# Optimization experiments

Measured on AMD Instinct MI355X. Metric: run time of the kernel, lower is better.

## Reference

```python
import jax, jax.numpy as jnp
import numpy as np
from jax import lax

B, P, K = 16, 1024, 32          # clouds, points per cloud, kNN neighbors
N = B * P
NCLS = 40
DIMS = [3, 64, 128, 256]


def setup_inputs() -> dict:
    key = jax.random.key(0)
    ks = jax.random.split(key, 16)
    inp = {
        "x": jax.random.normal(ks[0], (N, DIMS[0]), dtype=jnp.float32),
        "batch": jnp.repeat(jnp.arange(B, dtype=jnp.int64), P),
        "target": jax.random.randint(ks[1], (N,), 0, NCLS, dtype=jnp.int64),
    }
    for i, (fi, fo) in enumerate(zip(DIMS[:-1], DIMS[1:])):
        scale = 1.0 / np.sqrt(2 * fi)
        inp[f"W{i+1}"] = jax.random.normal(ks[2 + 2 * i], (2 * fi, fo), dtype=jnp.float32) * scale
        inp[f"b{i+1}"] = jnp.zeros((fo,), dtype=jnp.float32)
    inp["Wc"] = jax.random.normal(ks[10], (DIMS[-1], NCLS), dtype=jnp.float32) * (1.0 / np.sqrt(DIMS[-1]))
    inp["bc"] = jnp.zeros((NCLS,), dtype=jnp.float32)
    return inp


def knn_graph(x):
    """Per-cloud kNN (loop=False). x: [N,F] with nodes grouped in B clouds of P.
    Returns global neighbor indices [N, K]."""
    xb = x.reshape(B, P, -1)
    sq = jnp.sum(xb * xb, axis=-1)                       # [B,P]
    d2 = sq[:, :, None] + sq[:, None, :] - 2.0 * jnp.einsum("bpf,bqf->bpq", xb, xb)
    d2 = d2 + jnp.eye(P, dtype=x.dtype) * jnp.finfo(x.dtype).max  # exclude self-loops
    _, idx = lax.top_k(-d2, K)                           # [B,P,K] local indices
    gidx = idx + (jnp.arange(B) * P)[:, None, None]      # local -> global node ids
    return gidx.reshape(N, K)


def edge_conv(x, nbr, W, b):
    """EdgeConv: max_j MLP([x_i, x_j - x_i])."""
    xj = x[nbr]                                          # [N,K,F] gather
    xi = x[:, None, :]
    feat = jnp.concatenate([jnp.broadcast_to(xi, xj.shape), xj - xi], axis=-1)  # [N,K,2F]
    h = jnp.einsum("nkf,fo->nko", feat, W) + b           # [N,K,F']
    return jnp.max(h, axis=1)                            # max aggregation


def reference(x, batch, target, W1, b1, W2, b2, W3, b3, Wc, bc):
    del batch  # structure encoded as B clouds of P contiguous nodes
    for W, b in ((W1, b1), (W2, b2), (W3, b3)):
        nbr = knn_graph(x)                               # dynamic graph per layer
        x = jax.nn.relu(edge_conv(x, nbr, W, b))
    logits = x @ Wc + bc                                 # [N, NCLS]
    probs = jax.nn.softmax(logits, axis=-1)
    logp = jax.nn.log_softmax(logits, axis=-1)           # == probs.log()
    loss = -jnp.mean(jnp.take_along_axis(logp, target[:, None], axis=-1))
    return loss, probs
```

## Files before the change

### kernel.cpp

```cpp
#include <hip/hip_runtime.h>
#include <float.h>
#include <math.h>

#define BCLOUDS 16
#define PPTS    1024
#define NPTS    (BCLOUDS * PPTS)
#define KNB     32
#define NCLS    40
#define RPB     4
#define KNNBLK  (NPTS / RPB)
#define EDGEBLK (NPTS / 16)
#define NBINS   512
#define HWORDS  (NBINS / 2)
#define WPADW   (HWORDS + HWORDS / 16)
#define SELFM   0xFFFFFFFFu

__device__ __forceinline__ int widx(int w) { return w + (w >> 4); }

template<int F>
__global__ __launch_bounds__(256) void xpose_kernel(const float* __restrict__ x,
                                                    float* __restrict__ xT,
                                                    float* __restrict__ qn) {
    const int p = blockIdx.x * 256 + threadIdx.x;
    const int cloud = p >> 10, pl = p & 1023;
    const float* xr = x + (size_t)p * F;
    float* xTc = xT + (size_t)cloud * F * PPTS;
    float s = 0.f;
    for (int f = 0; f < F; ++f) {
        const float v = xr[f];
        s = fmaf(v, v, s);
        xTc[(size_t)f * PPTS + pl] = v;
    }
    qn[p] = s;
}

template<int F, int FO>
__global__ __launch_bounds__(256, 2) void knn_edge_kernel(const float* __restrict__ x,
                                                          const float* __restrict__ xT,
                                                          const float* __restrict__ qn,
                                                          int* __restrict__ nbr,
                                                          const float* __restrict__ W,
                                                          const float* __restrict__ bias,
                                                          float* __restrict__ A,
                                                          float* __restrict__ Bm) {
    __shared__ unsigned dmat[RPB][PPTS];
    __shared__ float    xp[RPB][F];
    __shared__ float    rn[RPB];
    __shared__ unsigned histw[RPB][WPADW];
    __shared__ float    xs[16][F];

    const int tid = threadIdx.x;

    if (blockIdx.x >= KNNBLK) {
        constexpr int RT  = 16;
        constexpr int RS  = 256 / FO;
        constexpr int RPT = RT / RS;
        const int n0 = (int)(blockIdx.x - KNNBLK) * RT;
        for (int i = tid; i < RT * F; i += 256)
            xs[i / F][i % F] = x[(size_t)n0 * F + i];
        __syncthreads();

        const int o  = tid % FO;
        const int r0 = tid / FO;
        float accA[RPT], accB[RPT];
#pragma unroll
        for (int i = 0; i < RPT; ++i) { accA[i] = 0.f; accB[i] = 0.f; }

        for (int f = 0; f < F; ++f) {
            const float wt = W[(size_t)f * FO + o];
            const float wb = W[(size_t)(F + f) * FO + o];
            const float wd = wt - wb;
#pragma unroll
            for (int i = 0; i < RPT; ++i) {
                const float xv = xs[r0 + i * RS][f];
                accA[i] = fmaf(xv, wd, accA[i]);
                accB[i] = fmaf(xv, wb, accB[i]);
            }
        }
        const float bo = bias[o];
#pragma unroll
        for (int i = 0; i < RPT; ++i) {
            const size_t row = (size_t)(n0 + r0 + i * RS);
            A[row * FO + o]  = accA[i] + bo;
            Bm[row * FO + o] = accB[i];
        }
        return;
    }

    const int lane  = tid & 63;
    const int wave  = tid >> 6;
    const int bid   = blockIdx.x;
    const int cloud = (bid & 7) + 8 * (bid >> 11);
    const int pl0   = ((bid >> 3) & 255) * RPB;

    const float* xc = x + (size_t)cloud * PPTS * F;
    for (int i = tid; i < RPB * F; i += 256)
        xp[i / F][i % F] = xc[(size_t)(pl0 + i / F) * F + (i % F)];
    __syncthreads();
    if (tid < RPB) {
        float s = 0.f;
        for (int f = 0; f < F; ++f) { const float v = xp[tid][f]; s = fmaf(v, v, s); }
        rn[tid] = s;
    }
    __syncthreads();

    const float* xTc = xT + (size_t)cloud * F * PPTS;
    const float4 qv = *reinterpret_cast<const float4*>(&qn[cloud * PPTS + 4 * tid]);

    float acc[RPB][4];
#pragma unroll
    for (int r = 0; r < RPB; ++r)
#pragma unroll
        for (int c = 0; c < 4; ++c) acc[r][c] = 0.f;

    if constexpr (F % 4 == 0) {
#pragma unroll 2
        for (int f4 = 0; f4 < F / 4; ++f4) {
            float4 vf[4];
#pragma unroll
            for (int j = 0; j < 4; ++j)
                vf[j] = *reinterpret_cast<const float4*>(&xTc[(size_t)(4 * f4 + j) * PPTS + 4 * tid]);
            float4 xr[RPB];
#pragma unroll
            for (int r = 0; r < RPB; ++r) xr[r] = *reinterpret_cast<const float4*>(&xp[r][4 * f4]);
#pragma unroll
            for (int r = 0; r < RPB; ++r) {
                acc[r][0] = fmaf(vf[0].x, xr[r].x, acc[r][0]);
                acc[r][1] = fmaf(vf[0].y, xr[r].x, acc[r][1]);
                acc[r][2] = fmaf(vf[0].z, xr[r].x, acc[r][2]);
                acc[r][3] = fmaf(vf[0].w, xr[r].x, acc[r][3]);
                acc[r][0] = fmaf(vf[1].x, xr[r].y, acc[r][0]);
                acc[r][1] = fmaf(vf[1].y, xr[r].y, acc[r][1]);
                acc[r][2] = fmaf(vf[1].z, xr[r].y, acc[r][2]);
                acc[r][3] = fmaf(vf[1].w, xr[r].y, acc[r][3]);
                acc[r][0] = fmaf(vf[2].x, xr[r].z, acc[r][0]);
                acc[r][1] = fmaf(vf[2].y, xr[r].z, acc[r][1]);
                acc[r][2] = fmaf(vf[2].z, xr[r].z, acc[r][2]);
                acc[r][3] = fmaf(vf[2].w, xr[r].z, acc[r][3]);
                acc[r][0] = fmaf(vf[3].x, xr[r].w, acc[r][0]);
                acc[r][1] = fmaf(vf[3].y, xr[r].w, acc[r][1]);
                acc[r][2] = fmaf(vf[3].z, xr[r].w, acc[r][2]);
                acc[r][3] = fmaf(vf[3].w, xr[r].w, acc[r][3]);
            }
        }
    } else {
        for (int f = 0; f < F; ++f) {
            const float4 v = *reinterpret_cast<const float4*>(&xTc[(size_t)f * PPTS + 4 * tid]);
#pragma unroll
            for (int r = 0; r < RPB; ++r) {
                const float xv = xp[r][f];
                acc[r][0] = fmaf(v.x, xv, acc[r][0]);
                acc[r][1] = fmaf(v.y, xv, acc[r][1]);
                acc[r][2] = fmaf(v.z, xv, acc[r][2]);
                acc[r][3] = fmaf(v.w, xv, acc[r][3]);
            }
        }
    }
#pragma unroll
    for (int r = 0; r < RPB; ++r) {
        uint4 wv;
        float d2;
        d2 = fmaxf(rn[r] + qv.x - 2.f * acc[r][0], 0.f);
        wv.x = (4 * tid + 0 == pl0 + r) ? SELFM : __float_as_uint(d2);
        d2 = fmaxf(rn[r] + qv.y - 2.f * acc[r][1], 0.f);
        wv.y = (4 * tid + 1 == pl0 + r) ? SELFM : __float_as_uint(d2);
        d2 = fmaxf(rn[r] + qv.z - 2.f * acc[r][2], 0.f);
        wv.z = (4 * tid + 2 == pl0 + r) ? SELFM : __float_as_uint(d2);
        d2 = fmaxf(rn[r] + qv.w - 2.f * acc[r][3], 0.f);
        wv.w = (4 * tid + 3 == pl0 + r) ? SELFM : __float_as_uint(d2);
        *reinterpret_cast<uint4*>(&dmat[r][4 * tid]) = wv;
    }
    __syncthreads();

    unsigned* hw = histw[wave];
    const int r = wave;
    const unsigned long long lmask = (1ull << lane) - 1ull;
    unsigned bits[16];
#pragma unroll
    for (int c = 0; c < 4; ++c) {
        const uint4 bv = *reinterpret_cast<const uint4*>(&dmat[r][4 * lane + 256 * c]);
        bits[4 * c + 0] = bv.x; bits[4 * c + 1] = bv.y;
        bits[4 * c + 2] = bv.z; bits[4 * c + 3] = bv.w;
    }

    unsigned m = bits[0];
#pragma unroll
    for (int i = 1; i < 16; ++i) m = min(m, bits[i]);
    unsigned gmin = m;
    unsigned tmax = (lane < 32) ? m : 0u;
#pragma unroll
    for (int off = 1; off < 64; off <<= 1) {
        gmin = min(gmin, (unsigned)__shfl_xor((int)gmin, off));
        tmax = max(tmax, (unsigned)__shfl_xor((int)tmax, off));
    }

    unsigned sm = 0u;
    int bsel = -1;
    int R = KNB;
    const unsigned base = gmin;
    int shift = 0;
    const bool have = tmax > gmin;
    if (have) {
        const unsigned span = tmax - gmin;
        const int lg = 31 - __clz(span);
        shift = lg > 8 ? lg - 8 : 0;
    }

    if (have) {
#pragma unroll
        for (int j = 0; j < 5; ++j) { const int k2 = lane + j * 64; if (k2 < WPADW) hw[k2] = 0u; }
#pragma unroll
        for (int i = 0; i < 16; ++i) {
            if (bits[i] <= tmax) {
                const int b = (int)((bits[i] - base) >> shift);
                atomicAdd(&hw[widx(b >> 1)], 1u << ((b & 1) << 4));
            }
        }
        unsigned h[8];
        int cnt = 0;
#pragma unroll
        for (int j = 0; j < 4; ++j) {
            const unsigned w = hw[widx(4 * lane + j)];
            h[2 * j]     = w & 0xFFFFu;
            h[2 * j + 1] = w >> 16;
            cnt += (int)(h[2 * j] + h[2 * j + 1]);
        }
        int pre = 0;
#pragma unroll
        for (int b = 0; b < 11; ++b) {
            const unsigned long long mk = __ballot((cnt >> b) & 1);
            pre += (int)__popcll(mk & lmask) << b;
        }
        const int inc = pre + cnt;
        const bool found = (pre < R && R <= inc);
        unsigned pk = 0;
        if (found) {
            int c = pre, bb = -1, cb = 0; unsigned hbv = 0;
#pragma unroll
            for (int j = 0; j < 8; ++j) {
                if (bb < 0) {
                    if (c + (int)h[j] >= R) { bb = lane * 8 + j; hbv = h[j]; cb = c; }
                    else c += (int)h[j];
                }
            }
            pk = (unsigned)bb | ((unsigned)cb << 9) | (hbv << 16);
        }
        const unsigned long long fm = __ballot(found);
        const int srcl = (int)__ffsll(fm) - 1;
        pk = (unsigned)__builtin_amdgcn_readlane((int)pk, srcl);
        const int bbin = (int)(pk & 511u);
        const int cb   = (int)((pk >> 9) & 127u);
        const int hb   = (int)(pk >> 16);
        const int need = R - cb;
        if (hb == need) {
            bsel = bbin + 1; R = 0;
        } else {
            bsel = bbin; R = need;
            unsigned nam = 0u;
#pragma unroll
            for (int i = 0; i < 16; ++i) {
                if (bits[i] <= tmax) {
                    const int b = (int)((bits[i] - base) >> shift);
                    if (b == bbin) nam |= 1u << i;
                }
            }
#pragma unroll 1
            while (R > 0) {
                unsigned lmin = 0xFFFFFFFFu;
#pragma unroll
                for (int i = 0; i < 16; ++i)
                    if ((nam >> i) & 1) lmin = min(lmin, bits[i]);
                unsigned vmin = lmin;
#pragma unroll
                for (int off = 1; off < 64; off <<= 1)
                    vmin = min(vmin, (unsigned)__shfl_xor((int)vmin, off));
                unsigned eq = 0u;
#pragma unroll
                for (int i = 0; i < 16; ++i)
                    if (((nam >> i) & 1) && bits[i] == vmin) eq |= 1u << i;
                const int ec = __popc(eq);
                int tot = 0;
#pragma unroll
                for (int b = 0; b < 5; ++b) {
                    const unsigned long long mk = __ballot((ec >> b) & 1);
                    tot += (int)__popcll(mk) << b;
                }
                if (tot <= R) {
                    sm |= eq; nam &= ~eq; R -= tot;
                } else {
#pragma unroll
                    for (int c = 0; c < 4; ++c) {
                        if (R > 0) {
                            const unsigned nib = (eq >> (4 * c)) & 0xFu;
                            const int cn = __popc(nib);
                            int prel = 0, totc = 0;
#pragma unroll
                            for (int b = 0; b < 3; ++b) {
                                const unsigned long long mk = __ballot((cn >> b) & 1);
                                prel += (int)__popcll(mk & lmask) << b;
                                totc += (int)__popcll(mk) << b;
                            }
                            int take = R - prel;
                            take = take < 0 ? 0 : (take > cn ? cn : take);
#pragma unroll
                            for (int j = 0; j < 4; ++j) {
                                if (((nib >> j) & 1) && take > 0) { sm |= 1u << (4 * c + j); --take; }
                            }
                            R -= totc < R ? totc : R;
                        }
                    }
                    R = 0;
                }
            }
        }
    } else {
        unsigned nam = 0u;
#pragma unroll
        for (int i = 0; i < 16; ++i) nam |= (bits[i] <= tmax) ? (1u << i) : 0u;
#pragma unroll
        for (int c = 0; c < 4; ++c) {
            if (R > 0) {
                const unsigned nib = (nam >> (4 * c)) & 0xFu;
                const int cn = __popc(nib);
                int prel = 0, totc = 0;
#pragma unroll
                for (int b = 0; b < 3; ++b) {
                    const unsigned long long mk = __ballot((cn >> b) & 1);
                    prel += (int)__popcll(mk & lmask) << b;
                    totc += (int)__popcll(mk) << b;
                }
                int take = R - prel;
                take = take < 0 ? 0 : (take > cn ? cn : take);
#pragma unroll
                for (int j = 0; j < 4; ++j) {
                    if (((nib >> j) & 1) && take > 0) { sm |= 1u << (4 * c + j); --take; }
                }
                R -= totc < R ? totc : R;
            }
        }
        R = 0;
    }

    int* out = nbr + (size_t)(cloud * PPTS + pl0 + r) * KNB;
    int slotbase = 0;
#pragma unroll
    for (int i = 0; i < 16; ++i) {
        bool sel = (sm >> i) & 1;
        if (bits[i] <= tmax) {
            const int b = (int)((bits[i] - base) >> shift);
            sel = sel || (b < bsel);
        }
        const unsigned long long mb = __ballot(sel);
        if (sel) {
            const int slot = slotbase + (int)__popcll(mb & lmask);
            if (slot < KNB) out[slot] = cloud * PPTS + 4 * lane + (i & 3) + 256 * (i >> 2);
        }
        slotbase += (int)__popcll(mb);
    }
    if (lane == 0)
        for (int s = slotbase; s < KNB; ++s) out[s] = cloud * PPTS + pl0 + r;
}

template<int FO>
__global__ __launch_bounds__(256) void combine_kernel(const float* __restrict__ A,
                                                      const float* __restrict__ Bm,
                                                      const int* __restrict__ nbr,
                                                      float* __restrict__ xout) {
    constexpr int FO4 = FO / 4;
    const int bid = (int)((blockIdx.x & 7) * (gridDim.x >> 3) + (blockIdx.x >> 3));
    const int idx = bid * 256 + threadIdx.x;
    const int n  = idx / FO4;
    const int o4 = idx % FO4;
    const int* nb = nbr + (size_t)n * KNB;
    const float4* B4 = reinterpret_cast<const float4*>(Bm);
    float4 mx = make_float4(-FLT_MAX, -FLT_MAX, -FLT_MAX, -FLT_MAX);
#pragma unroll 8
    for (int k = 0; k < KNB; ++k) {
        const float4 v = B4[(size_t)nb[k] * FO4 + o4];
        mx.x = fmaxf(mx.x, v.x); mx.y = fmaxf(mx.y, v.y);
        mx.z = fmaxf(mx.z, v.z); mx.w = fmaxf(mx.w, v.w);
    }
    const float4 a = reinterpret_cast<const float4*>(A)[idx];
    float4 rr;
    rr.x = fmaxf(a.x + mx.x, 0.f);
    rr.y = fmaxf(a.y + mx.y, 0.f);
    rr.z = fmaxf(a.z + mx.z, 0.f);
    rr.w = fmaxf(a.w + mx.w, 0.f);
    reinterpret_cast<float4*>(xout)[idx] = rr;
}

__global__ __launch_bounds__(320) void cls_gemm_kernel(const float* __restrict__ x,
                                                       const float* __restrict__ Wc,
                                                       const float* __restrict__ bc,
                                                       float* __restrict__ logits) {
    constexpr int RT = 16;
    __shared__ float xs[RT][256];
    __shared__ float wsm[256][NCLS];
    const int tid = threadIdx.x;
    const int n0  = blockIdx.x * RT;

    const float4* xsrc = reinterpret_cast<const float4*>(x + (size_t)n0 * 256);
    float4* xdst = reinterpret_cast<float4*>(&xs[0][0]);
    for (int i = tid; i < RT * 256 / 4; i += 320) xdst[i] = xsrc[i];
    for (int i = tid; i < 256 * NCLS; i += 320) wsm[i / NCLS][i % NCLS] = Wc[i];
    __syncthreads();

    const int o  = tid % NCLS;
    const int rg = tid / NCLS;
    float acc0 = 0.f, acc1 = 0.f;
#pragma unroll 4
    for (int f4 = 0; f4 < 64; ++f4) {
        float wv0 = wsm[4 * f4 + 0][o];
        float wv1 = wsm[4 * f4 + 1][o];
        float wv2 = wsm[4 * f4 + 2][o];
        float wv3 = wsm[4 * f4 + 3][o];
        const float4 xa = *reinterpret_cast<const float4*>(&xs[rg][4 * f4]);
        const float4 xb = *reinterpret_cast<const float4*>(&xs[rg + 8][4 * f4]);
        acc0 = fmaf(xa.x, wv0, acc0); acc0 = fmaf(xa.y, wv1, acc0);
        acc0 = fmaf(xa.z, wv2, acc0); acc0 = fmaf(xa.w, wv3, acc0);
        acc1 = fmaf(xb.x, wv0, acc1); acc1 = fmaf(xb.y, wv1, acc1);
        acc1 = fmaf(xb.z, wv2, acc1); acc1 = fmaf(xb.w, wv3, acc1);
    }
    const float bo = bc[o];
    logits[(size_t)(n0 + rg) * NCLS + o]     = acc0 + bo;
    logits[(size_t)(n0 + rg + 8) * NCLS + o] = acc1 + bo;
}

__global__ __launch_bounds__(256) void softmax_loss_kernel(const float* __restrict__ logits,
                                                           const int* __restrict__ target,
                                                           float* __restrict__ probs,
                                                           float* __restrict__ lossbuf) {
    const int tid = threadIdx.x;
    const int lane = tid & 63;
    const int n = blockIdx.x * 4 + (tid >> 6);
    float logit = -FLT_MAX;
    if (lane < NCLS) logit = logits[(size_t)n * NCLS + lane];
    float m = logit;
#pragma unroll
    for (int off = 32; off; off >>= 1) m = fmaxf(m, __shfl_xor(m, off));
    const float e = (lane < NCLS) ? __expf(logit - m) : 0.f;
    float s = e;
#pragma unroll
    for (int off = 32; off; off >>= 1) s += __shfl_xor(s, off);
    if (lane < NCLS) probs[(size_t)n * NCLS + lane] = e / s;
    const float lt = __shfl(logit, target[n]);
    if (lane == 0) lossbuf[n] = logf(s) - (lt - m);
}

__global__ __launch_bounds__(256) void loss_reduce_kernel(const float* __restrict__ lossbuf,
                                                          float* __restrict__ out) {
    __shared__ float s[256];
    float acc = 0.f;
    for (int i = threadIdx.x; i < NPTS; i += 256) acc += lossbuf[i];
    s[threadIdx.x] = acc;
    __syncthreads();
    for (int off = 128; off; off >>= 1) {
        if (threadIdx.x < off) s[threadIdx.x] += s[threadIdx.x + off];
        __syncthreads();
    }
    if (threadIdx.x == 0) out[0] = s[0] / (float)NPTS;
}

extern "C" void kernel_launch(void* const* d_in, const int* in_sizes, int n_in,
                              void* d_out, int out_size, void* d_ws, size_t ws_size,
                              hipStream_t stream) {
    (void)in_sizes; (void)n_in; (void)out_size; (void)ws_size;
    const float* x_in   = (const float*)d_in[0];
    const int*   target = (const int*)d_in[2];
    const float* W1 = (const float*)d_in[3];
    const float* b1 = (const float*)d_in[4];
    const float* W2 = (const float*)d_in[5];
    const float* b2 = (const float*)d_in[6];
    const float* W3 = (const float*)d_in[7];
    const float* b3 = (const float*)d_in[8];
    const float* Wc = (const float*)d_in[9];
    const float* bc = (const float*)d_in[10];

    char* ws = (char*)d_ws;
    float* X       = (float*)(ws);
    float* xT      = (float*)(ws + (size_t)8  * 1024 * 1024);
    float* A       = (float*)(ws + (size_t)16 * 1024 * 1024);
    float* Bm      = (float*)(ws + (size_t)32 * 1024 * 1024);
    int*   nbr     = (int*)  (ws + (size_t)48 * 1024 * 1024);
    float* lossbuf = (float*)(ws + (size_t)50 * 1024 * 1024);
    float* qn      = lossbuf;
    float* logits  = (float*)(ws + (size_t)16 * 1024 * 1024);

    float* outF  = (float*)d_out;
    float* probs = outF + 1;

    xpose_kernel<3><<<NPTS / 256, 256, 0, stream>>>(x_in, xT, qn);
    knn_edge_kernel<3, 64><<<KNNBLK + EDGEBLK, 256, 0, stream>>>(x_in, xT, qn, nbr, W1, b1, A, Bm);
    combine_kernel<64><<<NPTS * 16 / 256, 256, 0, stream>>>(A, Bm, nbr, X);

    xpose_kernel<64><<<NPTS / 256, 256, 0, stream>>>(X, xT, qn);
    knn_edge_kernel<64, 128><<<KNNBLK + EDGEBLK, 256, 0, stream>>>(X, xT, qn, nbr, W2, b2, A, Bm);
    combine_kernel<128><<<NPTS * 32 / 256, 256, 0, stream>>>(A, Bm, nbr, X);

    xpose_kernel<128><<<NPTS / 256, 256, 0, stream>>>(X, xT, qn);
    knn_edge_kernel<128, 256><<<KNNBLK + EDGEBLK, 256, 0, stream>>>(X, xT, qn, nbr, W3, b3, A, Bm);
    combine_kernel<256><<<NPTS * 64 / 256, 256, 0, stream>>>(A, Bm, nbr, X);

    cls_gemm_kernel<<<NPTS / 16, 320, 0, stream>>>(X, Wc, bc, logits);
    softmax_loss_kernel<<<NPTS / 4, 256, 0, stream>>>(logits, target, probs, lossbuf);
    loss_reduce_kernel<<<1, 256, 0, stream>>>(lossbuf, outF);
}
```

Baseline: 329.1 us.

## Sparse-candidate kNN selection with shared-memory slot counter and per-element tie break

Rewrites the per-row top-K selection so each lane keeps at most two candidate distances in registers and handles any further candidates by iterating a bitmask and re-reading them from shared memory. It drops the dense 16-way loops over all bits. The threshold-bin tie resolution now picks one element per iteration with a 64-bit (value, index) min-reduction. Output slots come from an LDS atomic counter instead of ballot prefix sums. This targets branch, ALU and ballot overhead in the selection, but adds serial per-element iterations in the tie loop and changes the order of neighbor indices in the output.

```diff
diff --git a/kernel.cpp b/kernel.cpp
--- a/kernel.cpp
+++ b/kernel.cpp
@@ -16,6 +16,7 @@
 #define SELFM   0xFFFFFFFFu
 
 __device__ __forceinline__ int widx(int w) { return w + (w >> 4); }
+__device__ __forceinline__ int slotq(int lane, int i) { return 4 * lane + (i & 3) + 256 * (i >> 2); }
 
 template<int F>
 __global__ __launch_bounds__(256) void xpose_kernel(const float* __restrict__ x,
@@ -47,6 +48,7 @@
     __shared__ float    xp[RPB][F];
     __shared__ float    rn[RPB];
     __shared__ unsigned histw[RPB][WPADW];
+    __shared__ unsigned slotctr[RPB];
     __shared__ float    xs[16][F];
 
     const int tid = threadIdx.x;
@@ -194,25 +196,41 @@
         tmax = max(tmax, (unsigned)__shfl_xor((int)tmax, off));
     }
 
-    unsigned sm = 0u;
+    unsigned act = 0u, v0 = 0u, v1 = 0u;
+    int i0 = -1, i1 = -1;
+#pragma unroll
+    for (int i = 0; i < 16; ++i) {
+        if (bits[i] <= tmax) {
+            act |= 1u << i;
+            if (i0 < 0)      { i0 = i; v0 = bits[i]; }
+            else if (i1 < 0) { i1 = i; v1 = bits[i]; }
+        }
+    }
+    unsigned ov = act & (act - 1); ov &= (ov - 1);
+
+    unsigned selm = 0u;
     int bsel = -1;
     int R = KNB;
     const unsigned base = gmin;
     int shift = 0;
     const bool have = tmax > gmin;
+    int b0 = -1, b1 = -1;
+
     if (have) {
         const unsigned span = tmax - gmin;
         const int lg = 31 - __clz(span);
         shift = lg > 8 ? lg - 8 : 0;
-    }
-
-    if (have) {
+
 #pragma unroll
         for (int j = 0; j < 5; ++j) { const int k2 = lane + j * 64; if (k2 < WPADW) hw[k2] = 0u; }
-#pragma unroll
-        for (int i = 0; i < 16; ++i) {
-            if (bits[i] <= tmax) {
-                const int b = (int)((bits[i] - base) >> shift);
+        if (i0 >= 0) { b0 = (int)((v0 - base) >> shift); atomicAdd(&hw[widx(b0 >> 1)], 1u << ((b0 & 1) << 4)); }
+        if (i1 >= 0) { b1 = (int)((v1 - base) >> shift); atomicAdd(&hw[widx(b1 >> 1)], 1u << ((b1 & 1) << 4)); }
+        {
+            unsigned t = ov;
+            while (t) {
+                const int i = __ffs(t) - 1; t &= t - 1;
+                const unsigned v = dmat[r][slotq(lane, i)];
+                const int b = (int)((v - base) >> shift);
                 atomicAdd(&hw[widx(b >> 1)], 1u << ((b & 1) << 4));
             }
         }
@@ -256,109 +274,92 @@
             bsel = bbin + 1; R = 0;
         } else {
             bsel = bbin; R = need;
-            unsigned nam = 0u;
-#pragma unroll
-            for (int i = 0; i < 16; ++i) {
-                if (bits[i] <= tmax) {
-                    const int b = (int)((bits[i] - base) >> shift);
-                    if (b == bbin) nam |= 1u << i;
+            unsigned bm = 0u;
+            if (b0 == bbin) bm |= 1u << i0;
+            if (b1 == bbin) bm |= 1u << i1;
+            {
+                unsigned t = ov;
+                while (t) {
+                    const int i = __ffs(t) - 1; t &= t - 1;
+                    const unsigned v = dmat[r][slotq(lane, i)];
+                    if ((int)((v - base) >> shift) == bbin) bm |= 1u << i;
                 }
             }
 #pragma unroll 1
             while (R > 0) {
-                unsigned lmin = 0xFFFFFFFFu;
-#pragma unroll
-                for (int i = 0; i < 16; ++i)
-                    if ((nam >> i) & 1) lmin = min(lmin, bits[i]);
-                unsigned vmin = lmin;
-#pragma unroll
-                for (int off = 1; off < 64; off <<= 1)
-                    vmin = min(vmin, (unsigned)__shfl_xor((int)vmin, off));
-                unsigned eq = 0u;
-#pragma unroll
-                for (int i = 0; i < 16; ++i)
-                    if (((nam >> i) & 1) && bits[i] == vmin) eq |= 1u << i;
-                const int ec = __popc(eq);
-                int tot = 0;
-#pragma unroll
-                for (int b = 0; b < 5; ++b) {
-                    const unsigned long long mk = __ballot((ec >> b) & 1);
-                    tot += (int)__popcll(mk) << b;
+                unsigned long long best = ~0ull;
+                unsigned t = bm;
+                while (t) {
+                    const int i = __ffs(t) - 1; t &= t - 1;
+                    const int q = slotq(lane, i);
+                    const unsigned v = dmat[r][q];
+                    const unsigned long long key = ((unsigned long long)v << 12) | (unsigned)q;
+                    best = best < key ? best : key;
                 }
-                if (tot <= R) {
-                    sm |= eq; nam &= ~eq; R -= tot;
-                } else {
-#pragma unroll
-                    for (int c = 0; c < 4; ++c) {
-                        if (R > 0) {
-                            const unsigned nib = (eq >> (4 * c)) & 0xFu;
-                            const int cn = __popc(nib);
-                            int prel = 0, totc = 0;
-#pragma unroll
-                            for (int b = 0; b < 3; ++b) {
-                                const unsigned long long mk = __ballot((cn >> b) & 1);
-                                prel += (int)__popcll(mk & lmask) << b;
-                                totc += (int)__popcll(mk) << b;
-                            }
-                            int take = R - prel;
-                            take = take < 0 ? 0 : (take > cn ? cn : take);
-#pragma unroll
-                            for (int j = 0; j < 4; ++j) {
-                                if (((nib >> j) & 1) && take > 0) { sm |= 1u << (4 * c + j); --take; }
-                            }
-                            R -= totc < R ? totc : R;
-                        }
-                    }
-                    R = 0;
+                unsigned long long gbest = best;
+#pragma unroll
+                for (int off = 1; off < 64; off <<= 1) {
+                    const unsigned long long o = __shfl_xor(gbest, off);
+                    gbest = o < gbest ? o : gbest;
                 }
+                const int qw = (int)(gbest & 0xFFFu);
+                if (((qw & 255) >> 2) == lane) {
+                    const int iw = ((qw >> 8) << 2) | (qw & 3);
+                    selm |= 1u << iw;
+                    bm &= ~(1u << iw);
+                }
+                --R;
             }
         }
     } else {
-        unsigned nam = 0u;
-#pragma unroll
-        for (int i = 0; i < 16; ++i) nam |= (bits[i] <= tmax) ? (1u << i) : 0u;
-#pragma unroll
-        for (int c = 0; c < 4; ++c) {
-            if (R > 0) {
-                const unsigned nib = (nam >> (4 * c)) & 0xFu;
-                const int cn = __popc(nib);
-                int prel = 0, totc = 0;
-#pragma unroll
-                for (int b = 0; b < 3; ++b) {
-                    const unsigned long long mk = __ballot((cn >> b) & 1);
-                    prel += (int)__popcll(mk & lmask) << b;
-                    totc += (int)__popcll(mk) << b;
-                }
-                int take = R - prel;
-                take = take < 0 ? 0 : (take > cn ? cn : take);
-#pragma unroll
-                for (int j = 0; j < 4; ++j) {
-                    if (((nib >> j) & 1) && take > 0) { sm |= 1u << (4 * c + j); --take; }
-                }
-                R -= totc < R ? totc : R;
-            }
-        }
-        R = 0;
-    }
-
+        unsigned bm = act;
+#pragma unroll 1
+        while (R > 0) {
+            const int il = __ffs(bm) - 1;
+            const int ql = (bm != 0u) ? slotq(lane, il) : 4096;
+            int gq = ql;
+#pragma unroll
+            for (int off = 1; off < 64; off <<= 1) gq = min(gq, __shfl_xor(gq, off));
+            if (ql == gq && bm != 0u) { selm |= 1u << il; bm &= ~(1u << il); }
+            --R;
+        }
+    }
+
+    if (lane == 0) slotctr[wave] = 0u;
     int* out = nbr + (size_t)(cloud * PPTS + pl0 + r) * KNB;
-    int slotbase = 0;
-#pragma unroll
-    for (int i = 0; i < 16; ++i) {
-        bool sel = (sm >> i) & 1;
-        if (bits[i] <= tmax) {
-            const int b = (int)((bits[i] - base) >> shift);
-            sel = sel || (b < bsel);
-        }
-        const unsigned long long mb = __ballot(sel);
+    if (i0 >= 0) {
+        const bool sel = ((selm >> i0) & 1) || (b0 >= 0 && b0 < bsel);
         if (sel) {
-            const int slot = slotbase + (int)__popcll(mb & lmask);
-            if (slot < KNB) out[slot] = cloud * PPTS + 4 * lane + (i & 3) + 256 * (i >> 2);
-        }
-        slotbase += (int)__popcll(mb);
-    }
+            const unsigned slot = atomicAdd(&slotctr[wave], 1u);
+            if (slot < KNB) out[slot] = cloud * PPTS + slotq(lane, i0);
+        }
+    }
+    if (i1 >= 0) {
+        const bool sel = ((selm >> i1) & 1) || (b1 >= 0 && b1 < bsel);
+        if (sel) {
+            const unsigned slot = atomicAdd(&slotctr[wave], 1u);
+            if (slot < KNB) out[slot] = cloud * PPTS + slotq(lane, i1);
+        }
+    }
+    {
+        unsigned t = ov;
+        while (t) {
+            const int i = __ffs(t) - 1; t &= t - 1;
+            const int q = slotq(lane, i);
+            bool sel = (selm >> i) & 1;
+            if (!sel && bsel > 0) {
+                const unsigned v = dmat[r][q];
+                sel = ((int)((v - base) >> shift) < bsel);
+            }
+            if (sel) {
+                const unsigned slot = atomicAdd(&slotctr[wave], 1u);
+                if (slot < KNB) out[slot] = cloud * PPTS + q;
+            }
+        }
+    }
+    const unsigned tot = slotctr[wave];
     if (lane == 0)
-        for (int s = slotbase; s < KNB; ++s) out[s] = cloud * PPTS + pl0 + r;
+        for (unsigned s = tot; s < KNB; ++s) out[s] = cloud * PPTS + pl0 + r;
 }
 
 template<int FO>
```

After: 323.3 us. About the same (-1.8%).
